# Performance work log

Hardware: AMD Instinct MI355X
Metric: run time of the kernel (lower is better)

The kernel has to match this reference:

```python
import jax, jax.numpy as jnp
import numpy as np

N = 50000      # nodes
E2 = 400000    # undirected edges
E = 2 * E2     # directed edges (each undirected edge in both directions)
DIN = 512      # input feature dim
DH = 128       # MLP hidden
C = 8          # num classes / BP channels


def setup_inputs() -> dict:
    key = jax.random.key(0)
    ks = jax.random.split(key, 9)
    x = jax.random.normal(ks[0], (N, DIN), jnp.float32)
    src0 = jax.random.randint(ks[1], (E2,), 0, N)
    dst0 = jax.random.randint(ks[2], (E2,), 0, N)
    # symmetric directed edge list: row 0 = source j, row 1 = target i
    edge_index = jnp.stack([jnp.concatenate([src0, dst0]),
                            jnp.concatenate([dst0, src0])])
    w0 = jax.random.uniform(ks[3], (E2,), jnp.float32, 0.5, 1.5)
    edge_weight = jnp.concatenate([w0, w0])  # reverse edge shares weight
    # edge_rv[e] = index of the reverse of edge e
    edge_rv = jnp.concatenate([jnp.arange(E2) + E2, jnp.arange(E2)])
    W1 = jax.random.normal(ks[4], (DIN, DH), jnp.float32) * 0.05
    b1 = jnp.zeros((DH,), jnp.float32)
    W2 = jax.random.normal(ks[5], (DH, C), jnp.float32) * 0.05
    b2 = jnp.zeros((C,), jnp.float32)
    param = jax.random.normal(ks[6], (C, C), jnp.float32) * 0.1
    return {"x": x, "edge_index": edge_index, "edge_weight": edge_weight,
            "edge_rv": edge_rv, "W1": W1, "b1": b1, "W2": W2, "b2": b2,
            "param": param, "K": 5}


def log_normalize(log_x):
    return log_x - jax.nn.logsumexp(log_x, axis=-1, keepdims=True)


def reference(x, edge_index, edge_weight, edge_rv, W1, b1, W2, b2, param, K):
    # MLP transform + LogSoftmax -> initial log-beliefs [N, C]
    h = jax.nn.relu(x @ W1 + b1)
    log_b0 = jax.nn.log_softmax(h @ W2 + b2, axis=-1)

    # learn_H=True: logH = logsigmoid(param + param^T), [C, C]
    logH = jax.nn.log_sigmoid(param + param.T)
    src, dst = edge_index[0], edge_index[1]
    # per-edge coupling matrix [E, C, C]
    logC = edge_weight[:, None, None] * logH[None, :, :]

    log_b = log_b0
    log_msg = None
    for _ in range(K):
        x_j = log_b[src]                       # gather source beliefs [E, C]
        if log_msg is not None:
            x_j = x_j - log_msg[edge_rv]       # remove reverse message
        # tropical-semiring matvec in log domain: logsumexp over source channel
        log_msg = log_normalize(jax.nn.logsumexp(x_j[:, :, None] + logC, axis=1))
        agg = jax.ops.segment_sum(log_msg, dst, num_segments=N)  # scatter-add
        log_b = log_normalize(log_b0 + agg)
    return log_b
```

## Files before the change

kernel.cpp:

```cpp
#include <hip/hip_runtime.h>
#include <hip/hip_bf16.h>
#include <hip/hip_fp16.h>
#include <math.h>

#define NN 50000
#define EE 800000
#define E2K 400000
#define DINK 512
#define DHK 128
#define CK 8
#define KIT 5
#define NBLKS 196
#define EPT 4

typedef __attribute__((ext_vector_type(8))) short short8;
typedef __attribute__((ext_vector_type(4))) float f32x4;

__device__ __forceinline__ unsigned short f2bf(float f) {
    union { float f; unsigned int u; } v;
    v.f = f;
    unsigned int u = v.u;
    unsigned int r = (u + 0x7FFFu + ((u >> 16) & 1u)) >> 16;
    return (unsigned short)r;
}
__device__ __forceinline__ float bfu2f(unsigned int lo16) {
    union { unsigned int u; float f; } v;
    v.u = lo16 << 16;
    return v.f;
}

__global__ __launch_bounds__(256) void prep_kernel(
    const float* __restrict__ W1, const float* __restrict__ param,
    unsigned short* __restrict__ W1t, float* __restrict__ logH,
    int* __restrict__ cnt) {
    if (blockIdx.x < 256) {
        int idx = blockIdx.x * 256 + threadIdx.x;
        int n = idx >> 9;
        int k = idx & 511;
        W1t[idx] = f2bf(W1[(size_t)k * DHK + n]);
    } else if (blockIdx.x == 256) {
        if (threadIdx.x < 64) {
            int t = threadIdx.x;
            int i = t >> 3, j = t & 7;
            float z = param[i * 8 + j] + param[j * 8 + i];
            logH[t] = fminf(z, 0.0f) - log1pf(expf(-fabsf(z)));
        }
    } else {
        int i = (blockIdx.x - 257) * 256 + threadIdx.x;
        if (i < NN) cnt[i] = 0;
    }
}

__device__ __forceinline__ void mlp_load(const float* const* xptr,
                                         const unsigned short* const* bptr,
                                         int koff, float4 (&ar)[4][2],
                                         short8 (&bc)[4]) {
#pragma unroll
    for (int mt = 0; mt < 4; ++mt) {
        ar[mt][0] = *(const float4*)(xptr[mt] + koff);
        ar[mt][1] = *(const float4*)(xptr[mt] + koff + 4);
    }
#pragma unroll
    for (int nt = 0; nt < 4; ++nt) bc[nt] = *(const short8*)(bptr[nt] + koff);
}

__device__ __forceinline__ void mlp_step(const float4 (&ar)[4][2],
                                         const short8 (&bc)[4],
                                         f32x4 (&acc)[4][4]) {
    short8 af[4];
#pragma unroll
    for (int mt = 0; mt < 4; ++mt) {
        union { short8 s; __hip_bfloat162 h[4]; } cv;
        cv.h[0] = __float22bfloat162_rn(make_float2(ar[mt][0].x, ar[mt][0].y));
        cv.h[1] = __float22bfloat162_rn(make_float2(ar[mt][0].z, ar[mt][0].w));
        cv.h[2] = __float22bfloat162_rn(make_float2(ar[mt][1].x, ar[mt][1].y));
        cv.h[3] = __float22bfloat162_rn(make_float2(ar[mt][1].z, ar[mt][1].w));
        af[mt] = cv.s;
    }
#pragma unroll
    for (int mt = 0; mt < 4; ++mt)
#pragma unroll
        for (int nt = 0; nt < 4; ++nt)
            acc[mt][nt] = __builtin_amdgcn_mfma_f32_16x16x32_bf16(
                af[mt], bc[nt], acc[mt][nt], 0, 0, 0);
}

__global__ __launch_bounds__(256) void mlp_mfma_kernel(
    const float* __restrict__ x, const unsigned short* __restrict__ W1t,
    const float* __restrict__ b1, const float* __restrict__ W2,
    const float* __restrict__ b2, float* __restrict__ logb0) {
    __shared__ unsigned short hs[128 * 136];
    __shared__ float W2s[128 * 8];
    __shared__ float b1s[128];
    __shared__ float b2s[8];

    const int tid = threadIdx.x;
    const int wave = tid >> 6;
    const int lane = tid & 63;
    const int q = lane >> 4;
    const int lm = lane & 15;
    const int wm = wave >> 1, wn = wave & 1;
    const int n0 = blockIdx.x * 128;

    if (tid < 128) b1s[tid] = b1[tid];
    if (tid < 8) b2s[tid] = b2[tid];
    {
        int i = tid * 4;
        *(float4*)&W2s[i] = *(const float4*)&W2[i];
    }
    __syncthreads();

    const float* xptr[4];
#pragma unroll
    for (int mt = 0; mt < 4; ++mt) {
        int r = n0 + wm * 64 + mt * 16 + lm;
        if (r > NN - 1) r = NN - 1;
        xptr[mt] = x + (size_t)r * DINK + q * 8;
    }
    const unsigned short* bptr[4];
#pragma unroll
    for (int nt = 0; nt < 4; ++nt) {
        int c = wn * 64 + nt * 16 + lm;
        bptr[nt] = W1t + (size_t)c * DINK + q * 8;
    }

    f32x4 acc[4][4];
#pragma unroll
    for (int mt = 0; mt < 4; ++mt)
#pragma unroll
        for (int nt = 0; nt < 4; ++nt) acc[mt][nt] = (f32x4){0.f, 0.f, 0.f, 0.f};

    float4 arA[4][2], arB[4][2];
    short8 bcA[4], bcB[4];
    mlp_load(xptr, bptr, 0, arA, bcA);
    mlp_load(xptr, bptr, 32, arB, bcB);

#pragma unroll
    for (int k0 = 0; k0 < DINK; k0 += 64) {
        mlp_step(arA, bcA, acc);
        if (k0 + 64 < DINK) mlp_load(xptr, bptr, k0 + 64, arA, bcA);
        mlp_step(arB, bcB, acc);
        if (k0 + 96 < DINK) mlp_load(xptr, bptr, k0 + 96, arB, bcB);
    }

#pragma unroll
    for (int nt = 0; nt < 4; ++nt) {
        int j = wn * 64 + nt * 16 + lm;
        float bj = b1s[j];
#pragma unroll
        for (int mt = 0; mt < 4; ++mt) {
            int rbase = wm * 64 + mt * 16 + q * 4;
#pragma unroll
            for (int r = 0; r < 4; ++r) {
                float h = fmaxf(acc[mt][nt][r] + bj, 0.0f);
                hs[(rbase + r) * 136 + j] = f2bf(h);
            }
        }
    }
    __syncthreads();

    int row = tid >> 1;
    int half = tid & 1;
    const unsigned short* hp = &hs[row * 136 + half * 64];
    float p[8] = {0.f, 0.f, 0.f, 0.f, 0.f, 0.f, 0.f, 0.f};
#pragma unroll
    for (int ch = 0; ch < 8; ++ch) {
        uint4 c4 = *(const uint4*)(hp + ch * 8);
        unsigned int uu[4] = {c4.x, c4.y, c4.z, c4.w};
#pragma unroll
        for (int p2 = 0; p2 < 4; ++p2) {
            float h0 = bfu2f(uu[p2] & 0xFFFFu);
            float h1 = bfu2f(uu[p2] >> 16);
            int j = half * 64 + ch * 8 + p2 * 2;
            const float* w0 = &W2s[j * 8];
            const float* w1 = &W2s[(j + 1) * 8];
#pragma unroll
            for (int c = 0; c < 8; ++c) p[c] = fmaf(h0, w0[c], p[c]);
#pragma unroll
            for (int c = 0; c < 8; ++c) p[c] = fmaf(h1, w1[c], p[c]);
        }
    }
#pragma unroll
    for (int c = 0; c < 8; ++c) p[c] += __shfl_xor(p[c], 1, 64);
    int grow = n0 + row;
    if (half == 0 && grow < NN) {
        float v[8];
        float mx = -1e30f;
#pragma unroll
        for (int c = 0; c < 8; ++c) {
            v[c] = p[c] + b2s[c];
            mx = fmaxf(mx, v[c]);
        }
        float s = 0.0f;
#pragma unroll
        for (int c = 0; c < 8; ++c) s += expf(v[c] - mx);
        float ln = mx + logf(s);
        float4* p0 = (float4*)&logb0[(size_t)grow * 8];
        p0[0] = make_float4(v[0] - ln, v[1] - ln, v[2] - ln, v[3] - ln);
        p0[1] = make_float4(v[4] - ln, v[5] - ln, v[6] - ln, v[7] - ln);
    }
}


__global__ __launch_bounds__(256) void deg_pair_kernel(const int* __restrict__ ei,
                                                       int* __restrict__ cnt) {
    int e = blockIdx.x * 256 + threadIdx.x;
    if (e >= E2K) return;
    int s = ei[e];
    int d = ei[EE + e];
    atomicAdd(&cnt[d], 1);
    atomicAdd(&cnt[s], 1);
}

__global__ __launch_bounds__(256) void scan_partial_kernel(
    const int* __restrict__ cnt, int* __restrict__ partial) {
    __shared__ int sd[256];
    int t = threadIdx.x;
    int i = blockIdx.x * 256 + t;
    sd[t] = (i < NN) ? cnt[i] : 0;
    __syncthreads();
#pragma unroll
    for (int s = 128; s > 0; s >>= 1) {
        if (t < s) sd[t] += sd[t + s];
        __syncthreads();
    }
    if (t == 0) partial[blockIdx.x] = sd[0];
}

__global__ __launch_bounds__(256) void scan_write2_kernel(
    const int* __restrict__ cnt, const int* __restrict__ partial,
    int* __restrict__ off, int* __restrict__ cnt_z) {
    __shared__ int sd[256];
    const int t = threadIdx.x;
    const int b = blockIdx.x;
    sd[t] = (t < NBLKS) ? partial[t] : 0;
    __syncthreads();
#pragma unroll
    for (int s = 1; s < 256; s <<= 1) {
        int a = sd[t];
        int v = (t >= s) ? sd[t - s] : 0;
        __syncthreads();
        sd[t] = a + v;
        __syncthreads();
    }
    const int top = (b > 0) ? sd[b - 1] : 0;
    __syncthreads();
    int i = b * 256 + t;
    int v = (i < NN) ? cnt[i] : 0;
    sd[t] = v;
    __syncthreads();
#pragma unroll
    for (int s = 1; s < 256; s <<= 1) {
        int a = sd[t];
        int w = (t >= s) ? sd[t - s] : 0;
        __syncthreads();
        sd[t] = a + w;
        __syncthreads();
    }
    if (i < NN) {
        off[i] = top + sd[t] - v;
        cnt_z[i] = 0;
    }
    if (i == NN - 1) off[NN] = EE;
}

__global__ __launch_bounds__(256) void pos_pair_kernel(
    const int* __restrict__ ei, const float* __restrict__ ew,
    const int* __restrict__ off, int* __restrict__ cnt,
    int2* __restrict__ perm_sw, int* __restrict__ rvp) {
    int e = blockIdx.x * 256 + threadIdx.x;
    if (e >= E2K) return;
    int s = ei[e];
    int d = ei[EE + e];
    int wbits = __float_as_int(ew[e]);
    int pA = off[d] + atomicAdd(&cnt[d], 1);
    int pB = off[s] + atomicAdd(&cnt[s], 1);
    int2 v;
    v.x = s; v.y = wbits; perm_sw[pA] = v;
    v.x = d;              perm_sw[pB] = v;
    rvp[pA] = pB;
    rvp[pB] = pA;
}

__global__ __launch_bounds__(256) void msg_kernel(
    const int2* __restrict__ perm_sw, const int* __restrict__ rvp,
    const float* __restrict__ logH, const uint4* __restrict__ msg_prev,
    const float* __restrict__ bel_prev, uint4* __restrict__ msg_next,
    int first) {
    __shared__ float lH[64];
    const int t = threadIdx.x;
    if (t < 64) lH[t] = logH[t];
    __syncthreads();

    const int base = blockIdx.x * (256 * EPT) + t;

    int jj[EPT];
    int2 sw[EPT];
    int rv[EPT];
#pragma unroll
    for (int e = 0; e < EPT; ++e) {
        int j = base + e * 256;
        jj[e] = j;
        int jc = (j < EE) ? j : (EE - 1);
        sw[e] = perm_sw[jc];
        rv[e] = rvp[jc];
    }

    const float* pb0 = &bel_prev[(size_t)sw[0].x * 8];
    float4 ba = *(const float4*)pb0;
    float4 bb = *(const float4*)(pb0 + 4);
    uint4 mp = make_uint4(0, 0, 0, 0);
    if (!first) mp = msg_prev[rv[0]];

#pragma unroll
    for (int e = 0; e < EPT; ++e) {
        float4 nba = ba, nbb = bb;
        uint4 nmp = mp;
        if (e + 1 < EPT) {
            const float* pb = &bel_prev[(size_t)sw[e + 1].x * 8];
            nba = *(const float4*)pb;
            nbb = *(const float4*)(pb + 4);
            if (!first) nmp = msg_prev[rv[e + 1]];
        }

        float w = __int_as_float(sw[e].y);
        float xj[8];
        xj[0] = ba.x; xj[1] = ba.y; xj[2] = ba.z; xj[3] = ba.w;
        xj[4] = bb.x; xj[5] = bb.y; xj[6] = bb.z; xj[7] = bb.w;
        if (!first) {
            union { uint4 u; _Float16 h[8]; } cv;
            cv.u = mp;
#pragma unroll
            for (int k = 0; k < 8; ++k) xj[k] -= (float)cv.h[k];
        }
        float mg[8];
#pragma unroll
        for (int c2 = 0; c2 < 8; ++c2) {
            float ssum = 0.0f;
#pragma unroll
            for (int c1 = 0; c1 < 8; ++c1)
                ssum += __expf(fmaf(w, lH[c1 * 8 + c2], xj[c1]));
            mg[c2] = __logf(ssum);
        }
        union { uint4 u; _Float16 h[8]; } ov;
#pragma unroll
        for (int k = 0; k < 8; ++k) ov.h[k] = (_Float16)mg[k];
        if (jj[e] < EE) msg_next[jj[e]] = ov.u;

        ba = nba; bb = nbb; mp = nmp;
    }
}

__global__ __launch_bounds__(256) void agg_kernel(
    const float* __restrict__ logb0, const int* __restrict__ off,
    const uint4* __restrict__ msg, float* __restrict__ bel_next,
    float* __restrict__ out, int last) {
    const int t = threadIdx.x;
    const int n = blockIdx.x * 32 + (t >> 3);
    const int c = t & 7;
    if (n >= NN) return;
    float a = logb0[(size_t)n * 8 + c];
    const int j0 = off[n];
    const int j1 = off[n + 1];
    const _Float16* mh = (const _Float16*)msg;
    float s0 = 0.f, s1 = 0.f, s2 = 0.f, s3 = 0.f;
    int j = j0;
    for (; j + 4 <= j1; j += 4) {
        s0 += (float)mh[(size_t)(j + 0) * 8 + c];
        s1 += (float)mh[(size_t)(j + 1) * 8 + c];
        s2 += (float)mh[(size_t)(j + 2) * 8 + c];
        s3 += (float)mh[(size_t)(j + 3) * 8 + c];
    }
    for (; j < j1; ++j) s0 += (float)mh[(size_t)j * 8 + c];
    a += (s0 + s1) + (s2 + s3);
    float mx = a;
#pragma unroll
    for (int s = 1; s < 8; s <<= 1) mx = fmaxf(mx, __shfl_xor(mx, s, 8));
    float sum = __expf(a - mx);
#pragma unroll
    for (int s = 1; s < 8; s <<= 1) sum += __shfl_xor(sum, s, 8);
    float v = a - (mx + __logf(sum));
    if (last) out[(size_t)n * 8 + c] = v;
    else bel_next[(size_t)n * 8 + c] = v;
}

extern "C" void kernel_launch(void* const* d_in, const int* in_sizes, int n_in,
                              void* d_out, int out_size, void* d_ws, size_t ws_size,
                              hipStream_t stream) {
    const float* x = (const float*)d_in[0];
    const int* ei = (const int*)d_in[1];
    const float* ew = (const float*)d_in[2];
    const float* W1 = (const float*)d_in[4];
    const float* b1 = (const float*)d_in[5];
    const float* W2 = (const float*)d_in[6];
    const float* b2 = (const float*)d_in[7];
    const float* param = (const float*)d_in[8];
    float* out = (float*)d_out;

    float* wsf = (float*)d_ws;
    float* logH = wsf;
    float* logb0 = logH + 64;
    uint4* msgA = (uint4*)(logb0 + (size_t)NN * 8);
    uint4* msgB = msgA + EE;
    int* off = (int*)(msgB + EE);
    int2* perm_sw = (int2*)(off + 50004);
    int* rvp = (int*)(perm_sw + EE);
    unsigned short* W1t = (unsigned short*)(rvp + EE);
    float* belA = (float*)(W1t + 65536);
    float* belB = belA + (size_t)NN * 8;
    int* cnt = (int*)msgA;
    int* partial = cnt + NN;

    const int ZB = (NN + 255) / 256;
    prep_kernel<<<257 + ZB, 256, 0, stream>>>(W1, param, W1t, logH, cnt);
    mlp_mfma_kernel<<<(NN + 127) / 128, 256, 0, stream>>>(x, W1t, b1, W2, b2,
                                                          logb0);

    const int E2B = (E2K + 255) / 256;
    deg_pair_kernel<<<E2B, 256, 0, stream>>>(ei, cnt);
    scan_partial_kernel<<<NBLKS, 256, 0, stream>>>(cnt, partial);
    scan_write2_kernel<<<NBLKS, 256, 0, stream>>>(cnt, partial, off, cnt);
    pos_pair_kernel<<<E2B, 256, 0, stream>>>(ei, ew, off, cnt, perm_sw, rvp);

    const int MB = (EE + 256 * EPT - 1) / (256 * EPT);
    const int AB = (NN + 31) / 32;
    uint4* msgs[2] = {msgA, msgB};
    float* bels[2] = {belA, belB};
    const float* bprev = logb0;
    for (int it = 0; it < KIT; ++it) {
        msg_kernel<<<MB, 256, 0, stream>>>(
            perm_sw, rvp, logH, msgs[(it + 1) & 1] , bprev,
            msgs[it & 1] , it == 0 ? 1 : 0);
        agg_kernel<<<AB, 256, 0, stream>>>(
            logb0, off, msgs[it & 1], bels[it & 1], out,
            it == KIT - 1 ? 1 : 0);
        bprev = bels[it & 1];
    }
}
```

Measured before the change: 442.7 us.

## Precompute per-edge cavity inputs in aggregation to make message gathers single-index

The aggregation kernel now writes, for each outgoing CSR slot, the fp16 cavity value (new belief minus that edge's incoming message) into a z buffer. The message kernel then does a single 16-byte gather through the reverse-edge index, instead of a belief gather plus a separate reverse-message gather. The perm/rvp arrays are merged into one (reverse position, weight) array, and a new init kernel fills z with the initial beliefs. This removes one random gather per edge and the double-buffered belief/message arrays. In exchange, the aggregation kernel does extra per-edge writes, and the cavity values are stored in fp16.

```diff
diff --git a/kernel.cpp b/kernel.cpp
--- a/kernel.cpp
+++ b/kernel.cpp
@@ -267,7 +267,7 @@
 __global__ __launch_bounds__(256) void pos_pair_kernel(
     const int* __restrict__ ei, const float* __restrict__ ew,
     const int* __restrict__ off, int* __restrict__ cnt,
-    int2* __restrict__ perm_sw, int* __restrict__ rvp) {
+    int2* __restrict__ rw) {
     int e = blockIdx.x * 256 + threadIdx.x;
     if (e >= E2K) return;
     int s = ei[e];
@@ -276,17 +276,26 @@
     int pA = off[d] + atomicAdd(&cnt[d], 1);
     int pB = off[s] + atomicAdd(&cnt[s], 1);
     int2 v;
-    v.x = s; v.y = wbits; perm_sw[pA] = v;
-    v.x = d;              perm_sw[pB] = v;
-    rvp[pA] = pB;
-    rvp[pB] = pA;
+    v.x = pB; v.y = wbits; rw[pA] = v;
+    v.x = pA;              rw[pB] = v;
+}
+
+__global__ __launch_bounds__(256) void zinit_kernel(
+    const float* __restrict__ logb0, const int* __restrict__ off,
+    _Float16* __restrict__ z) {
+    const int t = threadIdx.x;
+    const int n = blockIdx.x * 32 + (t >> 3);
+    const int c = t & 7;
+    if (n >= NN) return;
+    _Float16 v = (_Float16)logb0[(size_t)n * 8 + c];
+    const int j0 = off[n];
+    const int j1 = off[n + 1];
+    for (int j = j0; j < j1; ++j) z[(size_t)j * 8 + c] = v;
 }
 
 __global__ __launch_bounds__(256) void msg_kernel(
-    const int2* __restrict__ perm_sw, const int* __restrict__ rvp,
-    const float* __restrict__ logH, const uint4* __restrict__ msg_prev,
-    const float* __restrict__ bel_prev, uint4* __restrict__ msg_next,
-    int first) {
+    const int2* __restrict__ rw, const float* __restrict__ logH,
+    const uint4* __restrict__ zbuf, uint4* __restrict__ msg_next) {
     __shared__ float lH[64];
     const int t = threadIdx.x;
     if (t < 64) lH[t] = logH[t];
@@ -294,45 +303,25 @@
 
     const int base = blockIdx.x * (256 * EPT) + t;
 
-    int jj[EPT];
-    int2 sw[EPT];
-    int rv[EPT];
+    int2 h[EPT];
 #pragma unroll
     for (int e = 0; e < EPT; ++e) {
         int j = base + e * 256;
-        jj[e] = j;
         int jc = (j < EE) ? j : (EE - 1);
-        sw[e] = perm_sw[jc];
-        rv[e] = rvp[jc];
-    }
-
-    const float* pb0 = &bel_prev[(size_t)sw[0].x * 8];
-    float4 ba = *(const float4*)pb0;
-    float4 bb = *(const float4*)(pb0 + 4);
-    uint4 mp = make_uint4(0, 0, 0, 0);
-    if (!first) mp = msg_prev[rv[0]];
+        h[e] = rw[jc];
+    }
+    uint4 zv[EPT];
+#pragma unroll
+    for (int e = 0; e < EPT; ++e) zv[e] = zbuf[h[e].x];
 
 #pragma unroll
     for (int e = 0; e < EPT; ++e) {
-        float4 nba = ba, nbb = bb;
-        uint4 nmp = mp;
-        if (e + 1 < EPT) {
-            const float* pb = &bel_prev[(size_t)sw[e + 1].x * 8];
-            nba = *(const float4*)pb;
-            nbb = *(const float4*)(pb + 4);
-            if (!first) nmp = msg_prev[rv[e + 1]];
-        }
-
-        float w = __int_as_float(sw[e].y);
+        float w = __int_as_float(h[e].y);
+        union { uint4 u; _Float16 hh[8]; } cv;
+        cv.u = zv[e];
         float xj[8];
-        xj[0] = ba.x; xj[1] = ba.y; xj[2] = ba.z; xj[3] = ba.w;
-        xj[4] = bb.x; xj[5] = bb.y; xj[6] = bb.z; xj[7] = bb.w;
-        if (!first) {
-            union { uint4 u; _Float16 h[8]; } cv;
-            cv.u = mp;
-#pragma unroll
-            for (int k = 0; k < 8; ++k) xj[k] -= (float)cv.h[k];
-        }
+#pragma unroll
+        for (int k = 0; k < 8; ++k) xj[k] = (float)cv.hh[k];
         float mg[8];
 #pragma unroll
         for (int c2 = 0; c2 < 8; ++c2) {
@@ -342,18 +331,17 @@
                 ssum += __expf(fmaf(w, lH[c1 * 8 + c2], xj[c1]));
             mg[c2] = __logf(ssum);
         }
-        union { uint4 u; _Float16 h[8]; } ov;
-#pragma unroll
-        for (int k = 0; k < 8; ++k) ov.h[k] = (_Float16)mg[k];
-        if (jj[e] < EE) msg_next[jj[e]] = ov.u;
-
-        ba = nba; bb = nbb; mp = nmp;
+        union { uint4 u; _Float16 hh[8]; } ov;
+#pragma unroll
+        for (int k = 0; k < 8; ++k) ov.hh[k] = (_Float16)mg[k];
+        int j = base + e * 256;
+        if (j < EE) msg_next[j] = ov.u;
     }
 }
 
 __global__ __launch_bounds__(256) void agg_kernel(
     const float* __restrict__ logb0, const int* __restrict__ off,
-    const uint4* __restrict__ msg, float* __restrict__ bel_next,
+    const uint4* __restrict__ msg, _Float16* __restrict__ z,
     float* __restrict__ out, int last) {
     const int t = threadIdx.x;
     const int n = blockIdx.x * 32 + (t >> 3);
@@ -380,8 +368,12 @@
 #pragma unroll
     for (int s = 1; s < 8; s <<= 1) sum += __shfl_xor(sum, s, 8);
     float v = a - (mx + __logf(sum));
-    if (last) out[(size_t)n * 8 + c] = v;
-    else bel_next[(size_t)n * 8 + c] = v;
+    if (last) {
+        out[(size_t)n * 8 + c] = v;
+    } else {
+        for (int jj = j0; jj < j1; ++jj)
+            z[(size_t)jj * 8 + c] = (_Float16)(v - (float)mh[(size_t)jj * 8 + c]);
+    }
 }
 
 extern "C" void kernel_launch(void* const* d_in, const int* in_sizes, int n_in,
@@ -400,15 +392,12 @@
     float* wsf = (float*)d_ws;
     float* logH = wsf;
     float* logb0 = logH + 64;
-    uint4* msgA = (uint4*)(logb0 + (size_t)NN * 8);
-    uint4* msgB = msgA + EE;
-    int* off = (int*)(msgB + EE);
-    int2* perm_sw = (int2*)(off + 50004);
-    int* rvp = (int*)(perm_sw + EE);
-    unsigned short* W1t = (unsigned short*)(rvp + EE);
-    float* belA = (float*)(W1t + 65536);
-    float* belB = belA + (size_t)NN * 8;
-    int* cnt = (int*)msgA;
+    uint4* msgbuf = (uint4*)(logb0 + (size_t)NN * 8);
+    uint4* zbuf = msgbuf + EE;
+    int* off = (int*)(zbuf + EE);
+    int2* rw = (int2*)(off + 50004);
+    unsigned short* W1t = (unsigned short*)(rw + EE);
+    int* cnt = (int*)msgbuf;
     int* partial = cnt + NN;
 
     const int ZB = (NN + 255) / 256;
@@ -420,20 +409,16 @@
     deg_pair_kernel<<<E2B, 256, 0, stream>>>(ei, cnt);
     scan_partial_kernel<<<NBLKS, 256, 0, stream>>>(cnt, partial);
     scan_write2_kernel<<<NBLKS, 256, 0, stream>>>(cnt, partial, off, cnt);
-    pos_pair_kernel<<<E2B, 256, 0, stream>>>(ei, ew, off, cnt, perm_sw, rvp);
+    pos_pair_kernel<<<E2B, 256, 0, stream>>>(ei, ew, off, cnt, rw);
+
+    const int AB = (NN + 31) / 32;
+    zinit_kernel<<<AB, 256, 0, stream>>>(logb0, off, (_Float16*)zbuf);
 
     const int MB = (EE + 256 * EPT - 1) / (256 * EPT);
-    const int AB = (NN + 31) / 32;
-    uint4* msgs[2] = {msgA, msgB};
-    float* bels[2] = {belA, belB};
-    const float* bprev = logb0;
     for (int it = 0; it < KIT; ++it) {
-        msg_kernel<<<MB, 256, 0, stream>>>(
-            perm_sw, rvp, logH, msgs[(it + 1) & 1] , bprev,
-            msgs[it & 1] , it == 0 ? 1 : 0);
-        agg_kernel<<<AB, 256, 0, stream>>>(
-            logb0, off, msgs[it & 1], bels[it & 1], out,
-            it == KIT - 1 ? 1 : 0);
-        bprev = bels[it & 1];
-    }
-}
+        msg_kernel<<<MB, 256, 0, stream>>>(rw, logH, zbuf, msgbuf);
+        agg_kernel<<<AB, 256, 0, stream>>>(logb0, off, msgbuf,
+                                           (_Float16*)zbuf, out,
+                                           it == KIT - 1 ? 1 : 0);
+    }
+}
```

Measured after the change: 479.4 us. 8.3% more time.
